# Kernel optimization log

Measured on AMD Instinct MI355X. Metric: run time of the kernel, lower is better.

The kernel has to match this reference:

```python
import jax, jax.numpy as jnp
import numpy as np

N_HEADS = 16

def setup_inputs() -> dict:
    key = jax.random.key(0)
    ks = jax.random.split(key, 5)
    B, T, C = 4, 2048, 1024
    s = 0.02
    return {
        "x": jax.random.normal(ks[0], (B, T, C), jnp.float32),
        "W_attn": jax.random.normal(ks[1], (C, 3 * C), jnp.float32) * s,
        "b_attn": jax.random.normal(ks[2], (3 * C,), jnp.float32) * s,
        "W_proj": jax.random.normal(ks[3], (C, C), jnp.float32) * s,
        "b_proj": jax.random.normal(ks[4], (C,), jnp.float32) * s,
    }

def reference(x, W_attn, b_attn, W_proj, b_proj):
    B, T, C = x.shape
    H = N_HEADS
    D = C // H  # head dim
    qkv = x @ W_attn + b_attn                      # [B,T,3C]
    q, k, v = jnp.split(qkv, 3, axis=2)
    # [B,T,C] -> [B,H,T,D]
    q = q.reshape(B, T, H, D).transpose(0, 2, 1, 3)
    k = k.reshape(B, T, H, D).transpose(0, 2, 1, 3)
    v = v.reshape(B, T, H, D).transpose(0, 2, 1, 3)
    scale = 1.0 / jnp.sqrt(jnp.asarray(D, q.dtype))
    attn = jnp.einsum("bhqd,bhkd->bhqk", q, k) * scale  # [B,H,T,T]
    causal = jnp.tril(jnp.ones((T, T), bool))
    attn = jnp.where(causal[None, None], attn, -jnp.inf)
    attn = jax.nn.softmax(attn, axis=-1)
    y = jnp.einsum("bhqk,bhkd->bhqd", attn, v)          # [B,H,T,D]
    y = y.transpose(0, 2, 1, 3).reshape(B, T, C)
    return y @ W_proj + b_proj
```

## Files before the change

kernel.cpp:

```cpp
#include <hip/hip_runtime.h>

typedef __bf16 bf16x8 __attribute__((ext_vector_type(8)));
typedef float f32x4 __attribute__((ext_vector_type(4)));
typedef float f32x16 __attribute__((ext_vector_type(16)));
typedef unsigned short ushort8 __attribute__((ext_vector_type(8)));
typedef unsigned int uint4v __attribute__((ext_vector_type(4)));

__device__ __forceinline__ unsigned short f2bf(float f) {
  __bf16 b = (__bf16)f;
  return __builtin_bit_cast(unsigned short, b);
}
__device__ __forceinline__ float bf2f(unsigned short u) {
  unsigned int x = ((unsigned int)u) << 16;
  return __builtin_bit_cast(float, x);
}

#define GLOAD_LDS16(g, l)                                              \
  __builtin_amdgcn_global_load_lds(                                    \
      (const __attribute__((address_space(1))) void*)(g),              \
      (__attribute__((address_space(3))) void*)(l), 16, 0, 0)

__global__ __launch_bounds__(256) void f32_to_bf16_kernel(const float* __restrict__ in,
                                                          __bf16* __restrict__ out) {
  int i = blockIdx.x * 256 + threadIdx.x;
  const float4* p = (const float4*)(in + (size_t)i * 8);
  float4 f0 = p[0], f1 = p[1];
  ushort8 u = {f2bf(f0.x), f2bf(f0.y), f2bf(f0.z), f2bf(f0.w),
               f2bf(f1.x), f2bf(f1.y), f2bf(f1.z), f2bf(f1.w)};
  *(ushort8*)((unsigned short*)out + (size_t)i * 8) = u;
}

__global__ __launch_bounds__(256) void wtrans_kernel(const float* __restrict__ W,
                                                     __bf16* __restrict__ Wt,
                                                     int K, int N) {
  __shared__ float tile[32][33];
  int tx = threadIdx.x, ty = threadIdx.y;
  int n0 = blockIdx.x * 32, k0 = blockIdx.y * 32;
#pragma unroll
  for (int i = 0; i < 32; i += 8)
    tile[ty + i][tx] = W[(size_t)(k0 + ty + i) * N + n0 + tx];
  __syncthreads();
#pragma unroll
  for (int i = 0; i < 32; i += 8)
    Wt[(size_t)(n0 + ty + i) * K + k0 + tx] = (__bf16)tile[tx][ty + i];
}

template <int OUT_F32>
__global__ __launch_bounds__(256) void gemm_bt_kernel(const __bf16* __restrict__ Ab,
                                                      const __bf16* __restrict__ Bt,
                                                      const float* __restrict__ bias,
                                                      void* __restrict__ Cp,
                                                      int M, int N, int K) {
  __shared__ __align__(16) unsigned short As[128 * 32];
  __shared__ __align__(16) unsigned short Bs[128 * 32];
  const int tid = threadIdx.x;
  const int lane = tid & 63;
  const int wid = tid >> 6;
  const int lr = lane & 15, lg = lane >> 4;
  const int gx = gridDim.x;
  int nwg = gx * gridDim.y;
  int bid = blockIdx.y * gx + blockIdx.x;
  if ((nwg & 7) == 0) {
    int cpx = nwg >> 3;
    bid = (bid & 7) * cpx + (bid >> 3);
  }
  const int m0 = (bid / gx) * 128, n0 = (bid % gx) * 128;
  const int wm = (wid >> 1) * 64, wn = (wid & 1) * 64;
  const int sr = tid >> 2, sc = (tid & 3) * 8;
  const unsigned short* Ag = (const unsigned short*)Ab + (size_t)(m0 + sr) * K + sc;
  const unsigned short* Bg = (const unsigned short*)Bt + (size_t)(n0 + sr) * K + sc;
  f32x4 acc[4][4] = {};
  for (int k0 = 0; k0 < K; k0 += 32) {
    GLOAD_LDS16(Ag + k0, As + tid * 8);
    GLOAD_LDS16(Ag + (size_t)64 * K + k0, As + 2048 + tid * 8);
    GLOAD_LDS16(Bg + k0, Bs + tid * 8);
    GLOAD_LDS16(Bg + (size_t)64 * K + k0, Bs + 2048 + tid * 8);
    __syncthreads();
    bf16x8 af[4], bfr[4];
#pragma unroll
    for (int i = 0; i < 4; ++i) af[i] = *(const bf16x8*)&As[(wm + i * 16 + lr) * 32 + lg * 8];
#pragma unroll
    for (int i = 0; i < 4; ++i) bfr[i] = *(const bf16x8*)&Bs[(wn + i * 16 + lr) * 32 + lg * 8];
#pragma unroll
    for (int i = 0; i < 4; ++i)
#pragma unroll
      for (int jn = 0; jn < 4; ++jn)
        acc[i][jn] = __builtin_amdgcn_mfma_f32_16x16x32_bf16(af[i], bfr[jn], acc[i][jn], 0, 0, 0);
    __syncthreads();
  }
#pragma unroll
  for (int i = 0; i < 4; ++i)
#pragma unroll
    for (int jn = 0; jn < 4; ++jn)
#pragma unroll
      for (int jj = 0; jj < 4; ++jj) {
        int row = m0 + wm + i * 16 + lg * 4 + jj;
        int col = n0 + wn + jn * 16 + lr;
        float v = acc[i][jn][jj] + bias[col];
        if (OUT_F32)
          ((float*)Cp)[(size_t)row * N + col] = v;
        else
          ((unsigned short*)Cp)[(size_t)row * N + col] = f2bf(v);
      }
}

__global__ __launch_bounds__(256) void vtrans_kernel(const __bf16* __restrict__ qkv,
                                                     __bf16* __restrict__ Vt) {
  __shared__ __align__(16) unsigned short tile[64][72];
  int bh = blockIdx.y, b = bh >> 4, h = bh & 15;
  int t0 = blockIdx.x * 64;
  int tid = threadIdx.x;
#pragma unroll
  for (int p = 0; p < 2; ++p) {
    int idx = p * 256 + tid;
    int r = idx >> 3, c8 = (idx & 7) * 8;
    *(ushort8*)&tile[r][c8] = *(const ushort8*)((const unsigned short*)qkv +
                                                (size_t)(b * 2048 + t0 + r) * 3072 + 2048 +
                                                h * 64 + c8);
  }
  __syncthreads();
#pragma unroll
  for (int p = 0; p < 2; ++p) {
    int idx = p * 256 + tid;
    int d = idx >> 3, c8 = (idx & 7) * 8;
    ushort8 u;
#pragma unroll
    for (int i = 0; i < 8; ++i) u[i] = tile[c8 + i][d];
    *(ushort8*)((unsigned short*)Vt + (size_t)(bh * 64 + d) * 2048 + t0 + c8) = u;
  }
}

__global__ __launch_bounds__(256) void attn_kernel(const __bf16* __restrict__ qkvp,
                                                   const __bf16* __restrict__ Vt,
                                                   __bf16* __restrict__ yb) {
  __shared__ __align__(16) unsigned short Ks[2][64][72];
  __shared__ __align__(16) unsigned short Vs[2][64][72];
  const int bx = blockIdx.x;
  const int qb = 15 - (bx >> 6);
  const int bh = bx & 63;
  const int b = bh >> 4, h = bh & 15;
  const int tid = threadIdx.x, wid = tid >> 6, lane = tid & 63;
  const int lq = lane & 31, hi = lane >> 5;
  const unsigned short* qkv = (const unsigned short*)qkvp;
  const unsigned short* Vh = (const unsigned short*)Vt + (size_t)bh * 64 * 2048;
  const int q0w = qb * 128 + wid * 32;
  const int jmax_w = 2 * qb + (wid >> 1);
  const int qrel = (wid & 1) * 32 + lq;
  const int J = 2 * qb + 2;
  const int r0 = tid >> 3, r1 = 32 + (tid >> 3), c8 = (tid & 7) * 8;
  const unsigned short* Kcol = qkv + (size_t)b * 2048 * 3072 + 1024 + h * 64 + c8;

  const float qs = 0.125f * 1.44269504f;
  bf16x8 qf[4];
  {
    const unsigned short* Qg = qkv + (size_t)(b * 2048 + q0w + lq) * 3072 + h * 64;
#pragma unroll
    for (int dc = 0; dc < 4; ++dc) {
      ushort8 uq = *(const ushort8*)(Qg + dc * 16 + hi * 8);
      uint4v w;
#pragma unroll
      for (int i = 0; i < 4; ++i) {
        float lo = bf2f(uq[2 * i]) * qs;
        float hh = bf2f(uq[2 * i + 1]) * qs;
        unsigned int up;
        asm("v_cvt_pk_bf16_f32 %0, %1, %2" : "=v"(up) : "v"(lo), "v"(hh));
        w[i] = up;
      }
      qf[dc] = __builtin_bit_cast(bf16x8, w);
    }
  }

  f32x16 yacc[2] = {};
  float m_r = -1e30f, l_r = 0.f;

  ushort8 kr0, kr1, vr0, vr1;
  auto issue_loads = [&](int jt) {
    kr0 = *(const ushort8*)(Kcol + (size_t)(jt * 64 + r0) * 3072);
    kr1 = *(const ushort8*)(Kcol + (size_t)(jt * 64 + r1) * 3072);
    vr0 = *(const ushort8*)(Vh + (size_t)r0 * 2048 + jt * 64 + c8);
    vr1 = *(const ushort8*)(Vh + (size_t)r1 * 2048 + jt * 64 + c8);
  };
  auto write_tile = [&](int bi) {
    *(ushort8*)&Ks[bi][r0][c8] = kr0;
    *(ushort8*)&Ks[bi][r1][c8] = kr1;
    *(ushort8*)&Vs[bi][r0][c8] = vr0;
    *(ushort8*)&Vs[bi][r1][c8] = vr1;
  };

  issue_loads(0);
  write_tile(0);
  if (J > 1) issue_loads(1);

  for (int j = 0; j < J; ++j) {
    __syncthreads();
    const int cb = j & 1;
    if (j <= jmax_w) {
      f32x16 sa[2];
      __builtin_amdgcn_s_setprio(1);
#pragma unroll
      for (int kt32 = 0; kt32 < 2; ++kt32) {
        f32x16 s = {};
#pragma unroll
        for (int dc = 0; dc < 4; ++dc) {
          bf16x8 kf = *(const bf16x8*)&Ks[cb][kt32 * 32 + lq][dc * 16 + hi * 8];
          s = __builtin_amdgcn_mfma_f32_32x32x16_bf16(kf, qf[dc], s, 0, 0, 0);
        }
        sa[kt32] = s;
      }
      __builtin_amdgcn_s_setprio(0);
      if (j == jmax_w) {
#pragma unroll
        for (int kt32 = 0; kt32 < 2; ++kt32)
#pragma unroll
          for (int reg = 0; reg < 16; ++reg) {
            int kl = kt32 * 32 + (reg & 3) + 8 * (reg >> 2) + 4 * hi;
            if (kl > qrel) sa[kt32][reg] = -1e30f;
          }
      }
      float pmax = -1e30f;
#pragma unroll
      for (int kt32 = 0; kt32 < 2; ++kt32)
#pragma unroll
        for (int reg = 0; reg < 16; reg += 4)
          pmax = fmaxf(pmax, fmaxf(fmaxf(sa[kt32][reg], sa[kt32][reg + 1]),
                                   fmaxf(sa[kt32][reg + 2], sa[kt32][reg + 3])));
      pmax = fmaxf(pmax, __shfl_xor(pmax, 32));
      const bool need = __any(pmax > m_r + 8.f) != 0;
      const float mnew = need ? fmaxf(m_r, pmax) : m_r;
      const float alpha = exp2f(m_r - mnew);
      unsigned int u[2][8];
      float rs = 0.f;
#pragma unroll
      for (int kt32 = 0; kt32 < 2; ++kt32)
#pragma unroll
        for (int r = 0; r < 8; ++r) {
          float p0 = exp2f(sa[kt32][2 * r] - mnew);
          float p1 = exp2f(sa[kt32][2 * r + 1] - mnew);
          rs += p0 + p1;
          unsigned int up;
          asm("v_cvt_pk_bf16_f32 %0, %1, %2" : "=v"(up) : "v"(p0), "v"(p1));
          u[kt32][r] = up;
        }
      rs += __shfl_xor(rs, 32);
      l_r = l_r * alpha + rs;
      m_r = mnew;
      if (need) {
#pragma unroll
        for (int reg = 0; reg < 16; ++reg) {
          int row = (reg & 3) + 8 * (reg >> 2) + 4 * hi;
          float ac = __shfl(alpha, row);
          yacc[0][reg] *= ac;
          yacc[1][reg] *= ac;
        }
      }
      __builtin_amdgcn_s_setprio(1);
#pragma unroll
      for (int kt = 0; kt < 4; ++kt) {
        const int kt32 = kt >> 1, off = 4 * (kt & 1);
        unsigned int a0 = u[kt32][off + 0], a2 = u[kt32][off + 2];
        unsigned int a1 = u[kt32][off + 1], a3 = u[kt32][off + 3];
        asm("v_permlane32_swap_b32 %0, %1" : "+v"(a0), "+v"(a2));
        asm("v_permlane32_swap_b32 %0, %1" : "+v"(a1), "+v"(a3));
        uint4v pav = {a0, a1, a2, a3};
        bf16x8 paf = __builtin_bit_cast(bf16x8, pav);
#pragma unroll
        for (int dt = 0; dt < 2; ++dt) {
          bf16x8 vf = *(const bf16x8*)&Vs[cb][dt * 32 + lq][kt * 16 + hi * 8];
          yacc[dt] = __builtin_amdgcn_mfma_f32_32x32x16_bf16(paf, vf, yacc[dt], 0, 0, 0);
        }
      }
      __builtin_amdgcn_s_setprio(0);
    }
    if (j + 1 < J) {
      write_tile(cb ^ 1);
      if (j + 2 < J) issue_loads(j + 2);
    }
  }
#pragma unroll
  for (int reg = 0; reg < 16; ++reg) {
    int row = (reg & 3) + 8 * (reg >> 2) + 4 * hi;
    float linv = 1.f / __shfl(l_r, row);
    int qg = q0w + row;
#pragma unroll
    for (int dt = 0; dt < 2; ++dt) {
      float v = yacc[dt][reg] * linv;
      ((unsigned short*)yb)[(size_t)(b * 2048 + qg) * 1024 + h * 64 + dt * 32 + lq] = f2bf(v);
    }
  }
}

extern "C" void kernel_launch(void* const* d_in, const int* in_sizes, int n_in,
                              void* d_out, int out_size, void* d_ws, size_t ws_size,
                              hipStream_t stream) {
  const float* x = (const float*)d_in[0];
  const float* W_attn = (const float*)d_in[1];
  const float* b_attn = (const float*)d_in[2];
  const float* W_proj = (const float*)d_in[3];
  const float* b_proj = (const float*)d_in[4];
  float* out = (float*)d_out;
  char* ws = (char*)d_ws;

  size_t off = 0;
  __bf16* WtA = (__bf16*)(ws + off); off += (size_t)3072 * 1024 * 2;
  __bf16* WtP = (__bf16*)(ws + off); off += (size_t)1024 * 1024 * 2;
  __bf16* qkv = (__bf16*)(ws + off); off += (size_t)8192 * 3072 * 2;
  __bf16* Vtb = (__bf16*)(ws + off); off += (size_t)64 * 2048 * 64 * 2;
  __bf16* xyb = (__bf16*)(ws + off); off += (size_t)8192 * 1024 * 2;
  __bf16* xb = xyb;
  __bf16* yb = xyb;
  (void)ws_size; (void)in_sizes; (void)n_in; (void)out_size;

  f32_to_bf16_kernel<<<4096, 256, 0, stream>>>(x, xb);
  wtrans_kernel<<<dim3(3072 / 32, 1024 / 32), dim3(32, 8), 0, stream>>>(W_attn, WtA, 1024, 3072);
  wtrans_kernel<<<dim3(1024 / 32, 1024 / 32), dim3(32, 8), 0, stream>>>(W_proj, WtP, 1024, 1024);
  gemm_bt_kernel<0><<<dim3(24, 64), 256, 0, stream>>>(xb, WtA, b_attn, qkv, 8192, 3072, 1024);
  vtrans_kernel<<<dim3(32, 64), 256, 0, stream>>>(qkv, Vtb);
  attn_kernel<<<dim3(1024), 256, 0, stream>>>(qkv, Vtb, yb);
  gemm_bt_kernel<1><<<dim3(8, 64), 256, 0, stream>>>(yb, WtP, b_proj, out, 8192, 1024, 1024);
}
```

Measured before the change: 206.6 us.

## Pre-pack K per head and load attention tiles straight into LDS

Adds a reshape kernel that copies K out of the interleaved qkv buffer into a contiguous [B*H, T, 64] layout, so the attention kernel reads K tiles as dense 8 KB blocks instead of rows with a 3072-element stride. The attention loop also drops the register-staged prefetch, which kept loads two tiles ahead and wrote them to LDS after compute. It now loads the next tile directly into the alternate LDS buffer at the top of each iteration, before compute. This costs an extra kernel launch and an extra round trip of K through memory. The direct load-to-LDS copy may also expose global-load latency that the previous prefetch hid.

```diff
diff --git a/kernel.cpp b/kernel.cpp
--- a/kernel.cpp
+++ b/kernel.cpp
@@ -104,6 +104,18 @@
       }
 }
 
+__global__ __launch_bounds__(256) void reshape_k_kernel(const __bf16* __restrict__ qkv,
+                                                        __bf16* __restrict__ Ko) {
+  int tid = blockIdx.x * 256 + threadIdx.x;
+  int d8 = tid & 7;
+  int t = (tid >> 3) & 2047;
+  int h = (tid >> 14) & 15;
+  int b = tid >> 18;
+  size_t src = (size_t)(b * 2048 + t) * 3072 + 1024 + h * 64 + d8 * 8;
+  size_t dst = (size_t)((b * 16 + h) * 2048 + t) * 64 + d8 * 8;
+  *(ushort8*)((unsigned short*)Ko + dst) = *(const ushort8*)((const unsigned short*)qkv + src);
+}
+
 __global__ __launch_bounds__(256) void vtrans_kernel(const __bf16* __restrict__ qkv,
                                                      __bf16* __restrict__ Vt) {
   __shared__ __align__(16) unsigned short tile[64][72];
@@ -131,6 +143,7 @@
 }
 
 __global__ __launch_bounds__(256) void attn_kernel(const __bf16* __restrict__ qkvp,
+                                                   const __bf16* __restrict__ Kg,
                                                    const __bf16* __restrict__ Vt,
                                                    __bf16* __restrict__ yb) {
   __shared__ __align__(16) unsigned short Ks[2][64][72];
@@ -142,13 +155,12 @@
   const int tid = threadIdx.x, wid = tid >> 6, lane = tid & 63;
   const int lq = lane & 31, hi = lane >> 5;
   const unsigned short* qkv = (const unsigned short*)qkvp;
+  const unsigned short* Kh = (const unsigned short*)Kg + (size_t)bh * 2048 * 64;
   const unsigned short* Vh = (const unsigned short*)Vt + (size_t)bh * 64 * 2048;
   const int q0w = qb * 128 + wid * 32;
   const int jmax_w = 2 * qb + (wid >> 1);
   const int qrel = (wid & 1) * 32 + lq;
   const int J = 2 * qb + 2;
-  const int r0 = tid >> 3, r1 = 32 + (tid >> 3), c8 = (tid & 7) * 8;
-  const unsigned short* Kcol = qkv + (size_t)b * 2048 * 3072 + 1024 + h * 64 + c8;
 
   const float qs = 0.125f * 1.44269504f;
   bf16x8 qf[4];
@@ -173,28 +185,32 @@
   f32x16 yacc[2] = {};
   float m_r = -1e30f, l_r = 0.f;
 
-  ushort8 kr0, kr1, vr0, vr1;
-  auto issue_loads = [&](int jt) {
-    kr0 = *(const ushort8*)(Kcol + (size_t)(jt * 64 + r0) * 3072);
-    kr1 = *(const ushort8*)(Kcol + (size_t)(jt * 64 + r1) * 3072);
-    vr0 = *(const ushort8*)(Vh + (size_t)r0 * 2048 + jt * 64 + c8);
-    vr1 = *(const ushort8*)(Vh + (size_t)r1 * 2048 + jt * 64 + c8);
-  };
-  auto write_tile = [&](int bi) {
-    *(ushort8*)&Ks[bi][r0][c8] = kr0;
-    *(ushort8*)&Ks[bi][r1][c8] = kr1;
-    *(ushort8*)&Vs[bi][r0][c8] = vr0;
-    *(ushort8*)&Vs[bi][r1][c8] = vr1;
-  };
-
-  issue_loads(0);
-  write_tile(0);
-  if (J > 1) issue_loads(1);
+  {
+#pragma unroll
+    for (int p = 0; p < 2; ++p) {
+      int idx = p * 256 + tid;
+      int r = idx >> 3, c8 = (idx & 7) * 8;
+      *(ushort8*)&Ks[0][r][c8] = *(const ushort8*)(Kh + (size_t)r * 64 + c8);
+      *(ushort8*)&Vs[0][r][c8] = *(const ushort8*)(Vh + (size_t)r * 2048 + c8);
+    }
+  }
 
   for (int j = 0; j < J; ++j) {
     __syncthreads();
-    const int cb = j & 1;
+    if (j + 1 < J) {
+      int bi = (j + 1) & 1;
+#pragma unroll
+      for (int p = 0; p < 2; ++p) {
+        int idx = p * 256 + tid;
+        int r = idx >> 3, c8 = (idx & 7) * 8;
+        *(ushort8*)&Ks[bi][r][c8] =
+            *(const ushort8*)(Kh + (size_t)((j + 1) * 64 + r) * 64 + c8);
+        *(ushort8*)&Vs[bi][r][c8] =
+            *(const ushort8*)(Vh + (size_t)r * 2048 + (j + 1) * 64 + c8);
+      }
+    }
     if (j <= jmax_w) {
+      const int cb = j & 1;
       f32x16 sa[2];
       __builtin_amdgcn_s_setprio(1);
 #pragma unroll
@@ -271,10 +287,6 @@
       }
       __builtin_amdgcn_s_setprio(0);
     }
-    if (j + 1 < J) {
-      write_tile(cb ^ 1);
-      if (j + 2 < J) issue_loads(j + 2);
-    }
   }
 #pragma unroll
   for (int reg = 0; reg < 16; ++reg) {
@@ -304,6 +316,7 @@
   __bf16* WtA = (__bf16*)(ws + off); off += (size_t)3072 * 1024 * 2;
   __bf16* WtP = (__bf16*)(ws + off); off += (size_t)1024 * 1024 * 2;
   __bf16* qkv = (__bf16*)(ws + off); off += (size_t)8192 * 3072 * 2;
+  __bf16* Kb  = (__bf16*)(ws + off); off += (size_t)64 * 2048 * 64 * 2;
   __bf16* Vtb = (__bf16*)(ws + off); off += (size_t)64 * 2048 * 64 * 2;
   __bf16* xyb = (__bf16*)(ws + off); off += (size_t)8192 * 1024 * 2;
   __bf16* xb = xyb;
@@ -314,7 +327,8 @@
   wtrans_kernel<<<dim3(3072 / 32, 1024 / 32), dim3(32, 8), 0, stream>>>(W_attn, WtA, 1024, 3072);
   wtrans_kernel<<<dim3(1024 / 32, 1024 / 32), dim3(32, 8), 0, stream>>>(W_proj, WtP, 1024, 1024);
   gemm_bt_kernel<0><<<dim3(24, 64), 256, 0, stream>>>(xb, WtA, b_attn, qkv, 8192, 3072, 1024);
+  reshape_k_kernel<<<4096, 256, 0, stream>>>(qkv, Kb);
   vtrans_kernel<<<dim3(32, 64), 256, 0, stream>>>(qkv, Vtb);
-  attn_kernel<<<dim3(1024), 256, 0, stream>>>(qkv, Vtb, yb);
+  attn_kernel<<<dim3(1024), 256, 0, stream>>>(qkv, Kb, Vtb, yb);
   gemm_bt_kernel<1><<<dim3(8, 64), 256, 0, stream>>>(yb, WtP, b_proj, out, 8192, 1024, 1024);
 }
```

New measurement: 209.9 us. Within noise of the previous version (+1.6%).

## Write K head-contiguous from QKV GEMM and use 512-thread attention blocks

Applied to the files above, without the earlier changes.

The QKV GEMM epilogue now writes the K section into a separate head-major [B,H,T,D] buffer, so attention loads K tiles contiguously instead of with a 3072-element row stride. The attention kernel now uses 512 threads (8 waves, 256 query rows per block) and 512 blocks, so each K/V tile staged in LDS is shared by twice as many query rows. The register-prefetch software pipeline is replaced by direct global-to-LDS copies issued right after the barrier, and the setprio hints are removed. In exchange, the GEMM epilogue does scattered 2-byte stores for K, there is less load latency hiding, and fewer, larger blocks may balance the causal workload less evenly.

```diff
diff --git a/kernel.cpp b/kernel.cpp
--- a/kernel.cpp
+++ b/kernel.cpp
@@ -45,11 +45,12 @@
     Wt[(size_t)(n0 + ty + i) * K + k0 + tx] = (__bf16)tile[tx][ty + i];
 }
 
-template <int OUT_F32>
+template <int OUT_F32, int KSPLIT>
 __global__ __launch_bounds__(256) void gemm_bt_kernel(const __bf16* __restrict__ Ab,
                                                       const __bf16* __restrict__ Bt,
                                                       const float* __restrict__ bias,
                                                       void* __restrict__ Cp,
+                                                      __bf16* __restrict__ Kbp,
                                                       int M, int N, int K) {
   __shared__ __align__(16) unsigned short As[128 * 32];
   __shared__ __align__(16) unsigned short Bs[128 * 32];
@@ -88,6 +89,7 @@
         acc[i][jn] = __builtin_amdgcn_mfma_f32_16x16x32_bf16(af[i], bfr[jn], acc[i][jn], 0, 0, 0);
     __syncthreads();
   }
+  const bool isK = KSPLIT && (n0 >= 1024) && (n0 < 2048);
 #pragma unroll
   for (int i = 0; i < 4; ++i)
 #pragma unroll
@@ -97,10 +99,15 @@
         int row = m0 + wm + i * 16 + lg * 4 + jj;
         int col = n0 + wn + jn * 16 + lr;
         float v = acc[i][jn][jj] + bias[col];
-        if (OUT_F32)
+        if (OUT_F32) {
           ((float*)Cp)[(size_t)row * N + col] = v;
-        else
+        } else if (isK) {
+          int h = (col - 1024) >> 6, d = col & 63;
+          int bq = row >> 11, t = row & 2047;
+          ((unsigned short*)Kbp)[(size_t)((bq * 16 + h) * 2048 + t) * 64 + d] = f2bf(v);
+        } else {
           ((unsigned short*)Cp)[(size_t)row * N + col] = f2bf(v);
+        }
       }
 }
 
@@ -130,25 +137,26 @@
   }
 }
 
-__global__ __launch_bounds__(256) void attn_kernel(const __bf16* __restrict__ qkvp,
+__global__ __launch_bounds__(512) void attn_kernel(const __bf16* __restrict__ qkvp,
+                                                   const __bf16* __restrict__ Kg,
                                                    const __bf16* __restrict__ Vt,
                                                    __bf16* __restrict__ yb) {
   __shared__ __align__(16) unsigned short Ks[2][64][72];
   __shared__ __align__(16) unsigned short Vs[2][64][72];
   const int bx = blockIdx.x;
-  const int qb = 15 - (bx >> 6);
+  const int qb = 7 - (bx >> 6);
   const int bh = bx & 63;
   const int b = bh >> 4, h = bh & 15;
   const int tid = threadIdx.x, wid = tid >> 6, lane = tid & 63;
   const int lq = lane & 31, hi = lane >> 5;
   const unsigned short* qkv = (const unsigned short*)qkvp;
+  const unsigned short* Kh = (const unsigned short*)Kg + (size_t)bh * 2048 * 64;
   const unsigned short* Vh = (const unsigned short*)Vt + (size_t)bh * 64 * 2048;
-  const int q0w = qb * 128 + wid * 32;
-  const int jmax_w = 2 * qb + (wid >> 1);
+  const int q0w = qb * 256 + wid * 32;
+  const int jmax_w = 4 * qb + (wid >> 1);
   const int qrel = (wid & 1) * 32 + lq;
-  const int J = 2 * qb + 2;
-  const int r0 = tid >> 3, r1 = 32 + (tid >> 3), c8 = (tid & 7) * 8;
-  const unsigned short* Kcol = qkv + (size_t)b * 2048 * 3072 + 1024 + h * 64 + c8;
+  const int J = 4 * qb + 4;
+  const int r = tid >> 3, c8s = (tid & 7) * 8;
 
   const float qs = 0.125f * 1.44269504f;
   bf16x8 qf[4];
@@ -173,30 +181,21 @@
   f32x16 yacc[2] = {};
   float m_r = -1e30f, l_r = 0.f;
 
-  ushort8 kr0, kr1, vr0, vr1;
-  auto issue_loads = [&](int jt) {
-    kr0 = *(const ushort8*)(Kcol + (size_t)(jt * 64 + r0) * 3072);
-    kr1 = *(const ushort8*)(Kcol + (size_t)(jt * 64 + r1) * 3072);
-    vr0 = *(const ushort8*)(Vh + (size_t)r0 * 2048 + jt * 64 + c8);
-    vr1 = *(const ushort8*)(Vh + (size_t)r1 * 2048 + jt * 64 + c8);
-  };
-  auto write_tile = [&](int bi) {
-    *(ushort8*)&Ks[bi][r0][c8] = kr0;
-    *(ushort8*)&Ks[bi][r1][c8] = kr1;
-    *(ushort8*)&Vs[bi][r0][c8] = vr0;
-    *(ushort8*)&Vs[bi][r1][c8] = vr1;
-  };
-
-  issue_loads(0);
-  write_tile(0);
-  if (J > 1) issue_loads(1);
+  *(ushort8*)&Ks[0][r][c8s] = *(const ushort8*)(Kh + (size_t)r * 64 + c8s);
+  *(ushort8*)&Vs[0][r][c8s] = *(const ushort8*)(Vh + (size_t)r * 2048 + c8s);
 
   for (int j = 0; j < J; ++j) {
     __syncthreads();
-    const int cb = j & 1;
+    if (j + 1 < J) {
+      int bi = (j + 1) & 1;
+      *(ushort8*)&Ks[bi][r][c8s] =
+          *(const ushort8*)(Kh + (size_t)((j + 1) * 64 + r) * 64 + c8s);
+      *(ushort8*)&Vs[bi][r][c8s] =
+          *(const ushort8*)(Vh + (size_t)r * 2048 + (j + 1) * 64 + c8s);
+    }
     if (j <= jmax_w) {
+      const int cb = j & 1;
       f32x16 sa[2];
-      __builtin_amdgcn_s_setprio(1);
 #pragma unroll
       for (int kt32 = 0; kt32 < 2; ++kt32) {
         f32x16 s = {};
@@ -207,7 +206,6 @@
         }
         sa[kt32] = s;
       }
-      __builtin_amdgcn_s_setprio(0);
       if (j == jmax_w) {
 #pragma unroll
         for (int kt32 = 0; kt32 < 2; ++kt32)
@@ -233,13 +231,13 @@
 #pragma unroll
       for (int kt32 = 0; kt32 < 2; ++kt32)
 #pragma unroll
-        for (int r = 0; r < 8; ++r) {
-          float p0 = exp2f(sa[kt32][2 * r] - mnew);
-          float p1 = exp2f(sa[kt32][2 * r + 1] - mnew);
+        for (int rr = 0; rr < 8; ++rr) {
+          float p0 = exp2f(sa[kt32][2 * rr] - mnew);
+          float p1 = exp2f(sa[kt32][2 * rr + 1] - mnew);
           rs += p0 + p1;
           unsigned int up;
           asm("v_cvt_pk_bf16_f32 %0, %1, %2" : "=v"(up) : "v"(p0), "v"(p1));
-          u[kt32][r] = up;
+          u[kt32][rr] = up;
         }
       rs += __shfl_xor(rs, 32);
       l_r = l_r * alpha + rs;
@@ -253,7 +251,6 @@
           yacc[1][reg] *= ac;
         }
       }
-      __builtin_amdgcn_s_setprio(1);
 #pragma unroll
       for (int kt = 0; kt < 4; ++kt) {
         const int kt32 = kt >> 1, off = 4 * (kt & 1);
@@ -269,11 +266,6 @@
           yacc[dt] = __builtin_amdgcn_mfma_f32_32x32x16_bf16(paf, vf, yacc[dt], 0, 0, 0);
         }
       }
-      __builtin_amdgcn_s_setprio(0);
-    }
-    if (j + 1 < J) {
-      write_tile(cb ^ 1);
-      if (j + 2 < J) issue_loads(j + 2);
     }
   }
 #pragma unroll
@@ -304,6 +296,7 @@
   __bf16* WtA = (__bf16*)(ws + off); off += (size_t)3072 * 1024 * 2;
   __bf16* WtP = (__bf16*)(ws + off); off += (size_t)1024 * 1024 * 2;
   __bf16* qkv = (__bf16*)(ws + off); off += (size_t)8192 * 3072 * 2;
+  __bf16* Kb  = (__bf16*)(ws + off); off += (size_t)64 * 2048 * 64 * 2;
   __bf16* Vtb = (__bf16*)(ws + off); off += (size_t)64 * 2048 * 64 * 2;
   __bf16* xyb = (__bf16*)(ws + off); off += (size_t)8192 * 1024 * 2;
   __bf16* xb = xyb;
@@ -313,8 +306,8 @@
   f32_to_bf16_kernel<<<4096, 256, 0, stream>>>(x, xb);
   wtrans_kernel<<<dim3(3072 / 32, 1024 / 32), dim3(32, 8), 0, stream>>>(W_attn, WtA, 1024, 3072);
   wtrans_kernel<<<dim3(1024 / 32, 1024 / 32), dim3(32, 8), 0, stream>>>(W_proj, WtP, 1024, 1024);
-  gemm_bt_kernel<0><<<dim3(24, 64), 256, 0, stream>>>(xb, WtA, b_attn, qkv, 8192, 3072, 1024);
+  gemm_bt_kernel<0, 1><<<dim3(24, 64), 256, 0, stream>>>(xb, WtA, b_attn, qkv, Kb, 8192, 3072, 1024);
   vtrans_kernel<<<dim3(32, 64), 256, 0, stream>>>(qkv, Vtb);
-  attn_kernel<<<dim3(1024), 256, 0, stream>>>(qkv, Vtb, yb);
-  gemm_bt_kernel<1><<<dim3(8, 64), 256, 0, stream>>>(yb, WtP, b_proj, out, 8192, 1024, 1024);
-}
+  attn_kernel<<<dim3(512), 512, 0, stream>>>(qkv, Kb, Vtb, yb);
+  gemm_bt_kernel<1, 0><<<dim3(8, 64), 256, 0, stream>>>(yb, WtP, b_proj, out, nullptr, 8192, 1024, 1024);
+}
```

Measured after the change: 202.0 us. 2.2% less time.
